# Optimization experiments

Measured on AMD Instinct MI355X. Metric: run time of the kernel, lower is better.

The kernel has to match this reference:

```python
import jax, jax.numpy as jnp
import numpy as np

LAMB = 0.1
NEG = -1e30  # safe -inf surrogate (avoids nan in logaddexp chains)


def _ctc_nll(log_probs, labels2d, input_lengths, label_lengths):
    """Standard CTC negative log-likelihood (blank=0) via forward DP.
    log_probs: [B,T,V] log-softmaxed; labels2d: [B,L] padded; lengths: [B].
    """
    B, T, V = log_probs.shape
    L = labels2d.shape[1]
    S = 2 * L + 1  # extended label sequence: blank, l1, blank, l2, ...
    s = jnp.arange(S)
    lab_idx = jnp.minimum(s // 2, L - 1)
    ext = jnp.where((s % 2 == 0)[None, :], 0, labels2d[:, lab_idx])  # [B,S]
    ext_m2 = jnp.concatenate([jnp.full((B, 2), -1, ext.dtype), ext[:, :-2]], axis=1)
    # skip (s-2 -> s) allowed only for non-blank positions with different prev label
    allow = ((s % 2 == 1) & (s >= 2))[None, :] & (ext != ext_m2)  # [B,S]

    # emission log-probs gathered per extended position: [B,T,S]
    ext_b = jnp.broadcast_to(ext[:, None, :], (B, T, S))
    emit = jnp.take_along_axis(log_probs, ext_b, axis=2)

    alpha = jnp.full((B, S), NEG, log_probs.dtype)
    alpha = alpha.at[:, 0].set(emit[:, 0, 0]).at[:, 1].set(emit[:, 0, 1])

    def step(alpha, inp):
        emit_t, t = inp
        a1 = jnp.concatenate([jnp.full((B, 1), NEG, alpha.dtype), alpha[:, :-1]], axis=1)
        a2 = jnp.concatenate([jnp.full((B, 2), NEG, alpha.dtype), alpha[:, :-2]], axis=1)
        a2 = jnp.where(allow, a2, NEG)
        new = jnp.logaddexp(jnp.logaddexp(alpha, a1), a2) + emit_t
        # freeze alpha for sequences that already ended
        new = jnp.where((t < input_lengths)[:, None], new, alpha)
        return new, None

    emits = jnp.swapaxes(emit, 0, 1)[1:]          # [T-1,B,S]
    ts = jnp.arange(1, T)
    alpha, _ = jax.lax.scan(step, alpha, (emits, ts))

    end = 2 * label_lengths                        # final blank position per seq
    a_end = jnp.take_along_axis(alpha, end[:, None], axis=1)[:, 0]
    a_end1 = jnp.take_along_axis(alpha, jnp.maximum(end - 1, 0)[:, None], axis=1)[:, 0]
    return -jnp.logaddexp(a_end, a_end1)           # [B] NLL, warp-ctc convention


def reference(logits, labels, input_lengths, label_lengths):
    B, T, V = logits.shape
    labels2d = labels.reshape(B, -1)
    log_probs = jax.nn.log_softmax(logits, axis=-1)
    costs_ctc = _ctc_nll(log_probs, labels2d, input_lengths, label_lengths)
    # CRF denominator with fully-connected graph: logZ = sum_t logsumexp_v logits
    mask = jnp.arange(T)[None, :] < input_lengths[:, None]
    costs_den = jnp.sum(jnp.where(mask, jax.nn.logsumexp(logits, axis=2), 0.0), axis=1)
    costs_all = costs_den - (1.0 + LAMB) * costs_ctc
    costs = costs_all.sum() / B  # size_average=True
    return costs.reshape(1)


def setup_inputs() -> dict:
    key = jax.random.key(0)
    k1, k2, k3, k4 = jax.random.split(key, 4)
    B, T, V, L = 16, 800, 4000, 100
    logits = jax.random.normal(k1, (B, T, V), dtype=jnp.float32)
    labels = jax.random.randint(k2, (B * L,), 1, V)          # blank=0 excluded
    input_lengths = jax.random.randint(k3, (B,), 400, T + 1)  # >= 2L+1
    label_lengths = jax.random.randint(k4, (B,), 1, L + 1)
    return {"logits": logits, "labels": labels,
            "input_lengths": input_lengths, "label_lengths": label_lengths}
```

## Files before the change

### kernel.cpp

```cpp
#include <hip/hip_runtime.h>
#include <math.h>

constexpr int B = 16, T = 800, V = 4000, L = 100;
constexpr int EST = 104;
constexpr float LAMB = 0.1f;
constexpr float LN2 = 0.6931471805599453f;

typedef float f32x4 __attribute__((ext_vector_type(4)));

__global__ __launch_bounds__(256) void lse_emit_kernel(
        const float* __restrict__ logits, const int* __restrict__ labels,
        float* __restrict__ lse_arr, float* __restrict__ emit_all) {
    const int w = threadIdx.x >> 6, lane = threadIdx.x & 63;
    const int row = blockIdx.x * 4 + w;
    const int b = row / T;
    const float* __restrict__ rp = logits + (size_t)row * V;
    const f32x4* __restrict__ rp4 = (const f32x4*)rp;

    float m0 = -INFINITY, s0 = 0.f, m1 = -INFINITY, s1 = 0.f;
    for (int i = lane; i < 500; i += 64) {
        f32x4 x = __builtin_nontemporal_load(rp4 + i);
        float xm = fmaxf(fmaxf(x.x, x.y), fmaxf(x.z, x.w));
        float nm = fmaxf(m0, xm);
        s0 = s0 * __expf(m0 - nm)
           + __expf(x.x - nm) + __expf(x.y - nm)
           + __expf(x.z - nm) + __expf(x.w - nm);
        m0 = nm;
    }
    for (int i = 500 + lane; i < 1000; i += 64) {
        f32x4 x = __builtin_nontemporal_load(rp4 + i);
        float xm = fmaxf(fmaxf(x.x, x.y), fmaxf(x.z, x.w));
        float nm = fmaxf(m1, xm);
        s1 = s1 * __expf(m1 - nm)
           + __expf(x.x - nm) + __expf(x.y - nm)
           + __expf(x.z - nm) + __expf(x.w - nm);
        m1 = nm;
    }
    float m = fmaxf(m0, m1);
    float s = s0 * __expf(m0 - m) + s1 * __expf(m1 - m);
    #pragma unroll
    for (int k = 1; k < 64; k <<= 1) {
        float om = __shfl_xor(m, k);
        float os = __shfl_xor(s, k);
        float nm = fmaxf(m, om);
        s = s * __expf(m - nm) + os * __expf(om - nm);
        m = nm;
    }
    float lse = m + __logf(s);

    if (lane < L / 2) {
        int2 lab = *(const int2*)(labels + b * L + 2 * lane);
        float2 o = make_float2(__expf(rp[lab.x] - lse),
                               __expf(rp[lab.y] - lse));
        *(float2*)(emit_all + (size_t)row * EST + 2 * lane) = o;
    } else if (lane == 50) {
        emit_all[(size_t)row * EST + 100] = __expf(rp[0] - lse);
    } else if (lane == 51) {
        lse_arr[row] = lse;
    }
}

__device__ __forceinline__ float dpp_shr1(float x) {
    return __int_as_float(__builtin_amdgcn_update_dpp(
        0, __float_as_int(x), 0x138 , 0xF, 0xF, false));
}
__device__ __forceinline__ float wave_max63(float x) {
    int xi;
    xi = __float_as_int(x);
    x = fmaxf(x, __int_as_float(__builtin_amdgcn_update_dpp(xi, xi, 0x111, 0xF, 0xF, false)));
    xi = __float_as_int(x);
    x = fmaxf(x, __int_as_float(__builtin_amdgcn_update_dpp(xi, xi, 0x112, 0xF, 0xF, false)));
    xi = __float_as_int(x);
    x = fmaxf(x, __int_as_float(__builtin_amdgcn_update_dpp(xi, xi, 0x114, 0xF, 0xF, false)));
    xi = __float_as_int(x);
    x = fmaxf(x, __int_as_float(__builtin_amdgcn_update_dpp(xi, xi, 0x118, 0xF, 0xF, false)));
    xi = __float_as_int(x);
    x = fmaxf(x, __int_as_float(__builtin_amdgcn_update_dpp(xi, xi, 0x142, 0xF, 0xF, false)));
    xi = __float_as_int(x);
    x = fmaxf(x, __int_as_float(__builtin_amdgcn_update_dpp(xi, xi, 0x143, 0xF, 0xF, false)));
    return x;
}

#define DPSTEP(Q, R) do {                                            \
    float pa3 = dpp_shr1(a3);                                        \
    float n0 = (a0 + pa3) * (R);                                     \
    float n1 = (a1 + a0 + (allow1 ? pa3 : 0.f)) * (Q).x;             \
    float n2 = (a2 + a1) * (R);                                      \
    float n3 = (a3 + a2 + (allow3 ? a1 : 0.f)) * (Q).y;              \
    a0 = n0; a1 = n1; a2 = n2; a3 = n3; } while (0)

#define REFILL(Q, R, TC) do {                                        \
    int u_ = (TC); u_ = (u_ < len) ? u_ : (len - 1);                 \
    const float* er_ = eA + u_ * EST;                                \
    (Q) = *(const float2*)(er_ + loff);                              \
    (R) = er_[100]; } while (0)

#define RESCALE() do {                                               \
    a0 = v0 ? a0 : 0.f; a1 = v1 ? a1 : 0.f;                          \
    a2 = v2 ? a2 : 0.f; a3 = v3 ? a3 : 0.f;                          \
    float lm_ = fmaxf(fmaxf(a0, a1), fmaxf(a2, a3));                 \
    float wm_ = wave_max63(lm_);                                     \
    int wmb_ = __builtin_amdgcn_readlane(__float_as_int(wm_), 63);   \
    int eb_ = (wmb_ >> 23) & 0xFF;              \
    int hs_ = (100 - (eb_ - 127)) >> 1;              \
    float sc_ = ldexpf(1.0f, hs_);                                   \
    a0 = (a0 * sc_) * sc_; a1 = (a1 * sc_) * sc_;                    \
    a2 = (a2 * sc_) * sc_; a3 = (a3 * sc_) * sc_;                    \
    esc -= 2 * hs_; } while (0)

__global__ __launch_bounds__(64) void ctc_dp_kernel(
        const float* __restrict__ lse_arr, const float* __restrict__ emit_all,
        const int* __restrict__ labels, const int* __restrict__ in_len,
        const int* __restrict__ lab_len, float* __restrict__ costs) {
    const int b = blockIdx.x;
    const int l = threadIdx.x;
    const int len = in_len[b];
    const int lb = lab_len[b];

    float den = 0.f;
    for (int t = l; t < len; t += 64) den += lse_arr[b * T + t];
    #pragma unroll
    for (int k = 1; k < 64; k <<= 1) den += __shfl_xor(den, k);

    int lab0 = -1, lab1 = -2;
    if (l < L / 2) {
        int2 lab = *(const int2*)(labels + b * L + 2 * l);
        lab0 = lab.x; lab1 = lab.y;
    }
    int labm1 = __shfl_up(lab1, 1);
    const bool allow1 = (l >= 1) && (lab0 != labm1);
    const bool allow3 = (lab1 != lab0);
    const int loff = (l < L / 2) ? 2 * l : 0;
    const int endst = 2 * lb;
    const bool v0 = (4 * l     <= endst);
    const bool v1 = (4 * l + 1 <= endst);
    const bool v2 = (4 * l + 2 <= endst);
    const bool v3 = (4 * l + 3 <= endst);
    const float* __restrict__ eA = emit_all + (size_t)b * T * EST;

    int esc = -60;
    const float BOOST = 0x1p60f;
    float a0 = (l == 0) ? eA[100] * BOOST : 0.f;
    float a1 = (l == 0) ? eA[0]   * BOOST : 0.f;
    float a2 = 0.f, a3 = 0.f;

    float2 q0, q1, q2, q3, q4, q5, q6, q7;
    float  r0, r1, r2, r3, r4, r5, r6, r7;
    REFILL(q0, r0, 1); REFILL(q1, r1, 2); REFILL(q2, r2, 3); REFILL(q3, r3, 4);
    REFILL(q4, r4, 5); REFILL(q5, r5, 6); REFILL(q6, r6, 7); REFILL(q7, r7, 8);

    int t = 1;
    for (; t + 7 < len; t += 8) {
        DPSTEP(q0, r0); REFILL(q0, r0, t + 8);
        DPSTEP(q1, r1); REFILL(q1, r1, t + 9);
        DPSTEP(q2, r2); REFILL(q2, r2, t + 10);
        DPSTEP(q3, r3); REFILL(q3, r3, t + 11);
        DPSTEP(q4, r4); REFILL(q4, r4, t + 12);
        DPSTEP(q5, r5); REFILL(q5, r5, t + 13);
        DPSTEP(q6, r6); REFILL(q6, r6, t + 14);
        DPSTEP(q7, r7); REFILL(q7, r7, t + 15);
        RESCALE();
    }
    if (t < len) { DPSTEP(q0, r0); ++t; }
    if (t < len) { DPSTEP(q1, r1); ++t; }
    if (t < len) { DPSTEP(q2, r2); ++t; }
    if (t < len) { DPSTEP(q3, r3); ++t; }
    if (t < len) { DPSTEP(q4, r4); ++t; }
    if (t < len) { DPSTEP(q5, r5); ++t; }
    if (t < len) { DPSTEP(q6, r6); ++t; }

    __shared__ float sa[256];
    sa[4 * l] = a0; sa[4 * l + 1] = a1; sa[4 * l + 2] = a2; sa[4 * l + 3] = a3;
    __syncthreads();
    if (l == 0) {
        int end = endst;
        float sum = sa[end] + sa[end - 1];
        sum = fmaxf(sum, 1e-37f);
        float nll = -(logf(sum) + (float)esc * LN2);
        costs[b] = den - (1.0f + LAMB) * nll;
    }
}

__global__ void finalize_kernel(const float* __restrict__ costs,
                                float* __restrict__ out) {
    int tid = threadIdx.x;
    float c = (tid < B) ? costs[tid] : 0.f;
    #pragma unroll
    for (int off = 32; off > 0; off >>= 1) c += __shfl_down(c, off, 64);
    if (tid == 0) out[0] = c / (float)B;
}

extern "C" void kernel_launch(void* const* d_in, const int* in_sizes, int n_in,
                              void* d_out, int out_size, void* d_ws, size_t ws_size,
                              hipStream_t stream) {
    const float* logits  = (const float*)d_in[0];
    const int*   labels  = (const int*)d_in[1];
    const int*   in_len  = (const int*)d_in[2];
    const int*   lab_len = (const int*)d_in[3];
    float* out = (float*)d_out;

    float* emit_all = (float*)d_ws;
    float* lse_arr  = emit_all + (size_t)B * T * EST;
    float* costs    = lse_arr + B * T;

    lse_emit_kernel<<<B * T / 4, 256, 0, stream>>>(logits, labels, lse_arr, emit_all);
    ctc_dp_kernel<<<B, 64, 0, stream>>>(lse_arr, emit_all, labels, in_len, lab_len, costs);
    finalize_kernel<<<1, 64, 0, stream>>>(costs, out);
}
```

Before: 359.3 us.

## Stage emission rows into LDS via async global_load_lds ring buffer

Replaces the register-based 8-deep prefetch of emission rows in the CTC DP kernel with a 32-slot LDS ring buffer. Rows are filled by asynchronous global-to-LDS loads issued 24 steps ahead, with explicit vmcnt waits. The aim is to hide global memory latency on the serial time recurrence. The rescale factor is also built with bit manipulation instead of ldexpf. This relies on manual waitcnt counting and scheduling barriers, which is fragile if the compiler issues other memory operations.

After: 375.1 us. 1.04x slower.

```diff
diff --git a/kernel.cpp b/kernel.cpp
--- a/kernel.cpp
+++ b/kernel.cpp
@@ -89,11 +89,17 @@
     float n3 = (a3 + a2 + (allow3 ? a1 : 0.f)) * (Q).y;              \
     a0 = n0; a1 = n1; a2 = n2; a3 = n3; } while (0)
 
-#define REFILL(Q, R, TC) do {                                        \
-    int u_ = (TC); u_ = (u_ < len) ? u_ : (len - 1);                 \
-    const float* er_ = eA + u_ * EST;                                \
-    (Q) = *(const float2*)(er_ + loff);                              \
-    (R) = er_[100]; } while (0)
+#define STAGE_ROW(U) do {                                                     \
+    int u_ = (U); int uc_ = (u_ < len) ? u_ : (len - 1);                      \
+    const float* g0_ = eA + (size_t)uc_ * EST + l;                            \
+    float* l0_ = &smem[u_ & 31][0];                                           \
+    __builtin_amdgcn_global_load_lds(                                         \
+        (const __attribute__((address_space(1))) void*)g0_,                   \
+        (__attribute__((address_space(3))) void*)l0_, 4, 0, 0);               \
+    __builtin_amdgcn_global_load_lds(                                         \
+        (const __attribute__((address_space(1))) void*)(g0_ + 64),            \
+        (__attribute__((address_space(3))) void*)(l0_ + 64), 4, 0, 0);        \
+    } while (0)
 
 #define RESCALE() do {                                               \
     a0 = v0 ? a0 : 0.f; a1 = v1 ? a1 : 0.f;                          \
@@ -102,8 +108,8 @@
     float wm_ = wave_max63(lm_);                                     \
     int wmb_ = __builtin_amdgcn_readlane(__float_as_int(wm_), 63);   \
     int eb_ = (wmb_ >> 23) & 0xFF;              \
-    int hs_ = (100 - (eb_ - 127)) >> 1;              \
-    float sc_ = ldexpf(1.0f, hs_);                                   \
+    int hs_ = (100 - (eb_ - 127)) >> 1;        \
+    float sc_ = __int_as_float((127 + hs_) << 23);   \
     a0 = (a0 * sc_) * sc_; a1 = (a1 * sc_) * sc_;                    \
     a2 = (a2 * sc_) * sc_; a3 = (a3 * sc_) * sc_;                    \
     esc -= 2 * hs_; } while (0)
@@ -112,6 +118,8 @@
         const float* __restrict__ lse_arr, const float* __restrict__ emit_all,
         const int* __restrict__ labels, const int* __restrict__ in_len,
         const int* __restrict__ lab_len, float* __restrict__ costs) {
+    __shared__ float smem[32][128];
+    __shared__ float sa[256];
     const int b = blockIdx.x;
     const int l = threadIdx.x;
     const int len = in_len[b];
@@ -144,32 +152,39 @@
     float a1 = (l == 0) ? eA[0]   * BOOST : 0.f;
     float a2 = 0.f, a3 = 0.f;
 
-    float2 q0, q1, q2, q3, q4, q5, q6, q7;
-    float  r0, r1, r2, r3, r4, r5, r6, r7;
-    REFILL(q0, r0, 1); REFILL(q1, r1, 2); REFILL(q2, r2, 3); REFILL(q3, r3, 4);
-    REFILL(q4, r4, 5); REFILL(q5, r5, 6); REFILL(q6, r6, 7); REFILL(q7, r7, 8);
+    asm volatile("s_waitcnt vmcnt(0)" ::: "memory");
+    __builtin_amdgcn_sched_barrier(0);
+
+    #pragma unroll
+    for (int u = 1; u <= 24; ++u) STAGE_ROW(u);
 
     int t = 1;
     for (; t + 7 < len; t += 8) {
-        DPSTEP(q0, r0); REFILL(q0, r0, t + 8);
-        DPSTEP(q1, r1); REFILL(q1, r1, t + 9);
-        DPSTEP(q2, r2); REFILL(q2, r2, t + 10);
-        DPSTEP(q3, r3); REFILL(q3, r3, t + 11);
-        DPSTEP(q4, r4); REFILL(q4, r4, t + 12);
-        DPSTEP(q5, r5); REFILL(q5, r5, t + 13);
-        DPSTEP(q6, r6); REFILL(q6, r6, t + 14);
-        DPSTEP(q7, r7); REFILL(q7, r7, t + 15);
+        asm volatile("s_waitcnt vmcnt(32)" ::: "memory");
+        __builtin_amdgcn_sched_barrier(0);
+        #pragma unroll
+        for (int k = 0; k < 8; ++k) {
+            const int slot = (t + k) & 31;
+            float2 q = *(const float2*)&smem[slot][loff];
+            float  r = smem[slot][100];
+            DPSTEP(q, r);
+        }
         RESCALE();
-    }
-    if (t < len) { DPSTEP(q0, r0); ++t; }
-    if (t < len) { DPSTEP(q1, r1); ++t; }
-    if (t < len) { DPSTEP(q2, r2); ++t; }
-    if (t < len) { DPSTEP(q3, r3); ++t; }
-    if (t < len) { DPSTEP(q4, r4); ++t; }
-    if (t < len) { DPSTEP(q5, r5); ++t; }
-    if (t < len) { DPSTEP(q6, r6); ++t; }
-
-    __shared__ float sa[256];
+        __builtin_amdgcn_sched_barrier(0);
+        STAGE_ROW(t + 24); STAGE_ROW(t + 25);
+        STAGE_ROW(t + 26); STAGE_ROW(t + 27);
+        STAGE_ROW(t + 28); STAGE_ROW(t + 29);
+        STAGE_ROW(t + 30); STAGE_ROW(t + 31);
+    }
+    asm volatile("s_waitcnt vmcnt(0)" ::: "memory");
+    __builtin_amdgcn_sched_barrier(0);
+    for (; t < len; ++t) {
+        const int slot = t & 31;
+        float2 q = *(const float2*)&smem[slot][loff];
+        float  r = smem[slot][100];
+        DPSTEP(q, r);
+    }
+
     sa[4 * l] = a0; sa[4 * l + 1] = a1; sa[4 * l + 2] = a2; sa[4 * l + 3] = a3;
     __syncthreads();
     if (l == 0) {
```
